# Optimization experiments

Measured on AMD Instinct MI355X. Metric: run time of the kernel, lower is better.

Reference implementation:

```python
import jax, jax.numpy as jnp
import numpy as np

# Sizes
N, E = 100000, 3200000
F_NODE, F_EDGE, LD, HID, L = 4, 4, 6, 16, 8
ALPHA = 1.0
EPS = 1e-6


def setup_inputs() -> dict:
    key = jax.random.key(0)
    ks = jax.random.split(key, 8)
    x = jax.random.normal(ks[0], (N, F_NODE), jnp.float32)
    fixed_mask = jax.random.uniform(ks[1], (N,)) < 0.1
    x = x.at[:, -1].set(jnp.where(fixed_mask, jnp.abs(x[:, -1]) + 1.0, 0.0))
    # positive edge attributes (pipe resistance etc.)
    edge_attr = jax.random.uniform(ks[2], (E, F_EDGE), jnp.float32) * 0.9 + 0.1
    edge_index = jax.random.randint(ks[3], (2, E), 0, N, dtype=jnp.int64)
    d_in = 2 * LD + 2 * F_NODE + F_EDGE  # 24: [x_src, x_dst, attr_src, attr_dst, edge_attr]
    s = 0.1
    W1 = jax.random.normal(ks[4], (L, d_in, HID), jnp.float32) * s
    b1 = jnp.zeros((L, HID), jnp.float32)
    W2 = jax.random.normal(ks[5], (L, HID, LD), jnp.float32) * s
    b2 = jnp.zeros((L, LD), jnp.float32)
    Wf = jax.random.normal(ks[6], (LD, 1), jnp.float32) * s
    bf = jnp.zeros((1,), jnp.float32)
    return {"x": x, "edge_attr": edge_attr, "edge_index": edge_index,
            "W1": W1, "b1": b1, "W2": W2, "b2": b2, "Wf": Wf, "bf": bf}


def reference(x, edge_attr, edge_index, W1, b1, W2, b2, Wf, bf):
    src, dst = edge_index[0], edge_index[1]
    # in-degree for mean aggregation
    deg = jax.ops.segment_sum(jnp.ones((E,), jnp.float32), dst, num_segments=N)
    deg = jnp.maximum(deg, 1.0)
    X = jnp.zeros((N, LD), jnp.float32)
    na_src, na_dst = x[src], x[dst]  # static node-attr gathers reused each layer
    for l in range(L):  # num_convs GNNSConv layers
        m_in = jnp.concatenate([X[src], X[dst], na_src, na_dst, edge_attr], axis=-1)  # [E,24]
        h = jax.nn.relu(m_in @ W1[l] + b1[l])         # per-edge MLP hidden [E,16]
        m = h @ W2[l] + b2[l]                          # per-edge message [E,6]
        agg = jax.ops.segment_sum(m, dst, num_segments=N) / deg[:, None]  # mean aggr
        X = (1.0 - ALPHA) * X + ALPHA * agg            # latent update (alpha_update_x)
        X = jax.nn.relu(X)
    P = jax.nn.relu(X @ Wf + bf)                       # [N,1]
    fixed = x[:, -1]
    P_ = jnp.where(fixed != 0, fixed, P.reshape(-1))   # keep known pressures
    # BalanceConv: gas-network flow from squared-pressure drop, k = edge resistance
    dp2 = P_[src] ** 2 - P_[dst] ** 2
    k = edge_attr[:, 0]
    flows = jnp.sign(dp2) * jnp.sqrt(jnp.abs(dp2) / k + EPS)  # [E]
    inj = x[:, 0]  # nodal injection/demand
    balance = (jax.ops.segment_sum(flows, dst, num_segments=N)
               - jax.ops.segment_sum(flows, src, num_segments=N) + inj)
    imbalance = jnp.sqrt(jnp.sum(balance ** 2))
    return P, flows, jnp.stack([imbalance])
```

## Files before the change

### kernel.cpp

```cpp
#include <hip/hip_runtime.h>
#include <math.h>

#define N_NODES 100000
#define N_EDGES 3200000
#define F_NODE 4
#define F_EDGE 4
#define LD 6
#define HID 16
#define NLAYER 8
#define EPSF 1e-6f

#define NPB 64
#define NBK 1563
#define NBIN 196
#define G1 2000
#define CH (N_EDGES / G1)
#define TILE 2048

__device__ __forceinline__ unsigned f2bf(float a, float b) {
    unsigned ua = __float_as_uint(a);
    ua = (ua + 0x7fffu + ((ua >> 16) & 1u)) >> 16;
    unsigned ub = __float_as_uint(b);
    ub = (ub + 0x7fffu + ((ub >> 16) & 1u)) & 0xffff0000u;
    return ua | ub;
}
__device__ __forceinline__ float bflo(unsigned u) { return __uint_as_float(u << 16); }
__device__ __forceinline__ float bfhi(unsigned u) { return __uint_as_float(u & 0xffff0000u); }

__global__ __launch_bounds__(256) void hist_kernel(const int* __restrict__ ei,
                                                   int* __restrict__ ghd,
                                                   int* __restrict__ ghs) {
    __shared__ int hd[NBIN];
    __shared__ int hs[NBIN];
    int t = threadIdx.x, blk = blockIdx.x;
    for (int i = t; i < NBIN; i += 256) { hd[i] = 0; hs[i] = 0; }
    __syncthreads();
    int beg = blk * CH, end = beg + CH;
    for (int e = beg + t; e < end; e += 256) {
        atomicAdd(&hs[ei[e] >> 9], 1);
        atomicAdd(&hd[ei[N_EDGES + e] >> 9], 1);
    }
    __syncthreads();
    for (int i = t; i < NBIN; i += 256) {
        ghd[(size_t)i * G1 + blk] = hd[i];
        ghs[(size_t)i * G1 + blk] = hs[i];
    }
}

__global__ __launch_bounds__(256) void scanb_kernel(int* __restrict__ ghd, int* __restrict__ ghs,
                                                    int* __restrict__ totd, int* __restrict__ tots) {
    __shared__ int part[256];
    int b = blockIdx.x, t = threadIdx.x;
#pragma unroll
    for (int a = 0; a < 2; a++) {
        int* g = a ? ghs : ghd;
        int vals[8];
        int sum = 0;
#pragma unroll
        for (int k = 0; k < 8; k++) {
            int idx = t * 8 + k;
            vals[k] = (idx < G1) ? g[(size_t)b * G1 + idx] : 0;
            sum += vals[k];
        }
        part[t] = sum;
        __syncthreads();
        for (int off = 1; off < 256; off <<= 1) {
            int v = (t >= off) ? part[t - off] : 0;
            __syncthreads();
            part[t] += v;
            __syncthreads();
        }
        int excl = part[t] - sum;
#pragma unroll
        for (int k = 0; k < 8; k++) {
            int idx = t * 8 + k;
            if (idx < G1) g[(size_t)b * G1 + idx] = excl;
            excl += vals[k];
        }
        if (t == 0) (a ? tots : totd)[b] = part[255];
        __syncthreads();
    }
}

__global__ __launch_bounds__(256) void totscan_kernel(const int* __restrict__ totd,
                                                      const int* __restrict__ tots,
                                                      int* __restrict__ binbased,
                                                      int* __restrict__ binbases) {
    __shared__ int part[256];
    int t = threadIdx.x;
#pragma unroll
    for (int a = 0; a < 2; a++) {
        const int* tot = a ? tots : totd;
        int* base = a ? binbases : binbased;
        int v = (t < NBIN) ? tot[t] : 0;
        part[t] = v;
        __syncthreads();
        for (int off = 1; off < 256; off <<= 1) {
            int u = (t >= off) ? part[t - off] : 0;
            __syncthreads();
            part[t] += u;
            __syncthreads();
        }
        if (t < NBIN) base[t] = part[t] - v;
        if (t == 0) base[NBIN] = N_EDGES;
        __syncthreads();
    }
}

__global__ __launch_bounds__(256) void scatterA_kernel(const int* __restrict__ ei,
                                                       const int* __restrict__ ghd,
                                                       const int* __restrict__ ghs,
                                                       const int* __restrict__ binbased,
                                                       const int* __restrict__ binbases,
                                                       uint2* __restrict__ recA,
                                                       unsigned* __restrict__ sbufA) {
    __shared__ int curd[NBIN];
    __shared__ int curs[NBIN];
    int t = threadIdx.x, blk = blockIdx.x;
    for (int i = t; i < NBIN; i += 256) {
        curd[i] = binbased[i] + ghd[(size_t)i * G1 + blk];
        curs[i] = binbases[i] + ghs[(size_t)i * G1 + blk];
    }
    __syncthreads();
    int beg = blk * CH, end = beg + CH;
    for (int e = beg + t; e < end; e += 256) {
        int s = ei[e], d = ei[N_EDGES + e];
        int p = atomicAdd(&curd[d >> 9], 1);
        recA[p] = make_uint2((unsigned)s | ((unsigned)(d & 511) << 17), (unsigned)e);
        int q = atomicAdd(&curs[s >> 9], 1);
        sbufA[q] = (unsigned)e | ((unsigned)(s & 511) << 22);
    }
}

__global__ __launch_bounds__(256) void sortrec_kernel(const uint2* __restrict__ recA,
                                                      const float* __restrict__ ea,
                                                      const int* __restrict__ binbased,
                                                      uint4* __restrict__ recB,
                                                      float* __restrict__ degInv,
                                                      int* __restrict__ based_bk) {
    __shared__ int hist[512];
    __shared__ int cur[512];
    __shared__ int part[256];
    int b = blockIdx.x, t = threadIdx.x;
    hist[t] = 0;
    hist[t + 256] = 0;
    __syncthreads();
    int beg = binbased[b], end = binbased[b + 1];
    for (int i = beg + t; i < end; i += 256)
        atomicAdd(&hist[(recA[i].x >> 17) & 511u], 1);
    __syncthreads();
    int s0 = hist[2 * t], s1 = hist[2 * t + 1];
    int tsum = s0 + s1;
    part[t] = tsum;
    __syncthreads();
    for (int off = 1; off < 256; off <<= 1) {
        int v = (t >= off) ? part[t - off] : 0;
        __syncthreads();
        part[t] += v;
        __syncthreads();
    }
    int excl = part[t] - tsum;
    cur[2 * t] = beg + excl;
    cur[2 * t + 1] = beg + excl + s0;
    __syncthreads();
    int node0 = b << 9;
    for (int j = t; j < 512; j += 256) {
        int node = node0 + j;
        if (node < N_NODES) degInv[node] = 1.0f / fmaxf((float)hist[j], 1.0f);
    }
    if (t < 8) {
        int node = node0 + t * 64;
        if (node < N_NODES) based_bk[(b << 3) + t] = cur[t * 64];
    }
    if (b == NBIN - 1 && t == 0) based_bk[NBK] = N_EDGES;
    __syncthreads();
    for (int i = beg + t; i < end; i += 256) {
        uint2 r = recA[i];
        int nib = (int)((r.x >> 17) & 511u);
        unsigned s = r.x & 0x1FFFFu;
        unsigned e = r.y;
        int p = atomicAdd(&cur[nib], 1);
        float4 ev = reinterpret_cast<const float4*>(ea)[e];
        recB[p] = make_uint4(s | ((unsigned)(nib & 63) << 17),
                             f2bf(ev.x, ev.y), f2bf(ev.z, ev.w), e);
    }
}

__global__ __launch_bounds__(256) void sortsrc_kernel(const unsigned* __restrict__ sbufA,
                                                      const int* __restrict__ binbases,
                                                      unsigned* __restrict__ sbufB,
                                                      int* __restrict__ bases_bk) {
    __shared__ int hist[512];
    __shared__ int cur[512];
    __shared__ int part[256];
    int b = blockIdx.x, t = threadIdx.x;
    hist[t] = 0;
    hist[t + 256] = 0;
    __syncthreads();
    int beg = binbases[b], end = binbases[b + 1];
    for (int i = beg + t; i < end; i += 256)
        atomicAdd(&hist[(sbufA[i] >> 22) & 511u], 1);
    __syncthreads();
    int s0 = hist[2 * t], s1 = hist[2 * t + 1];
    int tsum = s0 + s1;
    part[t] = tsum;
    __syncthreads();
    for (int off = 1; off < 256; off <<= 1) {
        int v = (t >= off) ? part[t - off] : 0;
        __syncthreads();
        part[t] += v;
        __syncthreads();
    }
    int excl = part[t] - tsum;
    cur[2 * t] = beg + excl;
    cur[2 * t + 1] = beg + excl + s0;
    __syncthreads();
    if (t < 8) {
        int node = (b << 9) + t * 64;
        if (node < N_NODES) bases_bk[(b << 3) + t] = cur[t * 64];
    }
    if (b == NBIN - 1 && t == 0) bases_bk[NBK] = N_EDGES;
    __syncthreads();
    for (int i = beg + t; i < end; i += 256) {
        unsigned w = sbufA[i];
        int nib = (int)((w >> 22) & 511u);
        int p = atomicAdd(&cur[nib], 1);
        sbufB[p] = (w & 0x3FFFFFu) | ((unsigned)(nib & 63) << 22);
    }
}

__global__ __launch_bounds__(256) void ab_init(const float* __restrict__ x,
                                               const float* __restrict__ W1,
                                               const float* __restrict__ b1,
                                               unsigned* __restrict__ A,
                                               unsigned* __restrict__ B) {
    __shared__ float sW[8 * HID];
    __shared__ float sb[HID];
    int t = threadIdx.x;
    for (int i = t; i < 8 * HID; i += 256) sW[i] = W1[12 * HID + i];
    if (t < HID) sb[t] = b1[t];
    __syncthreads();
    int i = blockIdx.x * 256 + t;
    if (i >= N_NODES) return;
    float4 xv = reinterpret_cast<const float4*>(x)[i];
    float xf[4] = {xv.x, xv.y, xv.z, xv.w};
    float a[HID], bb[HID];
#pragma unroll
    for (int j = 0; j < HID; j++) { a[j] = sb[j]; bb[j] = 0.0f; }
#pragma unroll
    for (int r = 0; r < 4; r++) {
        float v = xf[r];
#pragma unroll
        for (int j = 0; j < HID; j++) {
            a[j]  = fmaf(v, sW[r * HID + j], a[j]);
            bb[j] = fmaf(v, sW[(4 + r) * HID + j], bb[j]);
        }
    }
    uint4* Ao = reinterpret_cast<uint4*>(A + (size_t)i * 8);
    Ao[0] = make_uint4(f2bf(a[0], a[1]), f2bf(a[2], a[3]), f2bf(a[4], a[5]), f2bf(a[6], a[7]));
    Ao[1] = make_uint4(f2bf(a[8], a[9]), f2bf(a[10], a[11]), f2bf(a[12], a[13]), f2bf(a[14], a[15]));
    uint4* Bo = reinterpret_cast<uint4*>(B + (size_t)i * 8);
    Bo[0] = make_uint4(f2bf(bb[0], bb[1]), f2bf(bb[2], bb[3]), f2bf(bb[4], bb[5]), f2bf(bb[6], bb[7]));
    Bo[1] = make_uint4(f2bf(bb[8], bb[9]), f2bf(bb[10], bb[11]), f2bf(bb[12], bb[13]), f2bf(bb[14], bb[15]));
}

template <int LAST>
__global__ __launch_bounds__(256) void edge_layer(const uint4* __restrict__ recB,
                                                  const unsigned* __restrict__ Ain,
                                                  const unsigned* __restrict__ Bin,
                                                  const float* __restrict__ x,
                                                  const float* __restrict__ degInv,
                                                  const float* __restrict__ W1l,
                                                  const float* __restrict__ W2l,
                                                  const float* __restrict__ b2l,
                                                  const float* __restrict__ W1n,
                                                  const float* __restrict__ b1n,
                                                  const float* __restrict__ Wf,
                                                  const float* __restrict__ bfp,
                                                  const int* __restrict__ based_bk,
                                                  unsigned* __restrict__ Aout,
                                                  unsigned* __restrict__ Bout,
                                                  float* __restrict__ Pout,
                                                  float* __restrict__ Pbuf) {
    __shared__ float sWea[4 * HID];
    __shared__ float sW2[HID * LD];
    __shared__ float sb2[LD];
    __shared__ float sW1n[20 * HID];
    __shared__ float sb1n[HID];
    __shared__ float sWf[LD];
    __shared__ float sbf;
    __shared__ float accf[LD * NPB];
    __shared__ unsigned sB[NPB * 8];
    __shared__ uint4 tile[TILE];
    int t = threadIdx.x;
    int b = blockIdx.x;
    for (int i = t; i < 4 * HID; i += 256) sWea[i] = W1l[20 * HID + i];
    for (int i = t; i < HID * LD; i += 256) sW2[i] = W2l[i];
    if (t < LD) sb2[t] = b2l[t];
    if (!LAST) {
        for (int i = t; i < 20 * HID; i += 256) sW1n[i] = W1n[i];
        if (t < HID) sb1n[t] = b1n[t];
    } else {
        if (t < LD) sWf[t] = Wf[t];
        if (t == 0) sbf = bfp[0];
    }
    for (int i = t; i < LD * NPB; i += 256) accf[i] = 0.0f;
    {
        size_t base8 = (size_t)(b << 6) * 8;
        for (int i = t; i < NPB * 8; i += 256) {
            size_t gi = base8 + i;
            sB[i] = (gi < (size_t)N_NODES * 8) ? Bin[gi] : 0u;
        }
    }
    __syncthreads();

    int beg = based_bk[b], end = based_bk[b + 1];

    for (int base = beg; base < end; base += TILE) {
        int m = end - base;
        if (m > TILE) m = TILE;
        for (int i = t; i < m; i += 256) tile[i] = recB[base + i];
        __syncthreads();
        int K2 = (m + 255) >> 8;
        int q0 = t * K2;
        int q1 = q0 + K2;
        if (q1 > m) q1 = m;
        float acc[LD];
        int cur = -1;
        uint4 bx, by;
#pragma unroll
        for (int o = 0; o < LD; o++) acc[o] = 0.0f;
#pragma unroll 2
        for (int q = q0; q < q1; ++q) {
            uint4 r = tile[q];
            int dl = (int)((r.x >> 17) & 63u);
            if (dl != cur) {
                if (cur >= 0) {
#pragma unroll
                    for (int o = 0; o < LD; o++) atomicAdd(&accf[o * NPB + cur], acc[o]);
                }
                cur = dl;
#pragma unroll
                for (int o = 0; o < LD; o++) acc[o] = 0.0f;
                const uint4* Bp = reinterpret_cast<const uint4*>(sB) + dl * 2;
                bx = Bp[0];
                by = Bp[1];
            }
            int s = (int)(r.x & 0x1FFFFu);
            const uint4* Ap = reinterpret_cast<const uint4*>(Ain + (size_t)s * 8);
            uint4 ax = Ap[0], ay = Ap[1];
            float h[HID];
            h[0]  = bflo(ax.x) + bflo(bx.x);  h[1]  = bfhi(ax.x) + bfhi(bx.x);
            h[2]  = bflo(ax.y) + bflo(bx.y);  h[3]  = bfhi(ax.y) + bfhi(bx.y);
            h[4]  = bflo(ax.z) + bflo(bx.z);  h[5]  = bfhi(ax.z) + bfhi(bx.z);
            h[6]  = bflo(ax.w) + bflo(bx.w);  h[7]  = bfhi(ax.w) + bfhi(bx.w);
            h[8]  = bflo(ay.x) + bflo(by.x);  h[9]  = bfhi(ay.x) + bfhi(by.x);
            h[10] = bflo(ay.y) + bflo(by.y);  h[11] = bfhi(ay.y) + bfhi(by.y);
            h[12] = bflo(ay.z) + bflo(by.z);  h[13] = bfhi(ay.z) + bfhi(by.z);
            h[14] = bflo(ay.w) + bflo(by.w);  h[15] = bfhi(ay.w) + bfhi(by.w);
            float ef[4] = {bflo(r.y), bfhi(r.y), bflo(r.z), bfhi(r.z)};
#pragma unroll
            for (int rr = 0; rr < 4; rr++) {
                float v = ef[rr];
#pragma unroll
                for (int j = 0; j < HID; j++) h[j] = fmaf(v, sWea[rr * HID + j], h[j]);
            }
#pragma unroll
            for (int j = 0; j < HID; j++) h[j] = fmaxf(h[j], 0.0f);
            float mo[LD];
#pragma unroll
            for (int o = 0; o < LD; o++) mo[o] = sb2[o];
#pragma unroll
            for (int j = 0; j < HID; j++) {
                float hj = h[j];
#pragma unroll
                for (int o = 0; o < LD; o++) mo[o] = fmaf(hj, sW2[j * LD + o], mo[o]);
            }
#pragma unroll
            for (int o = 0; o < LD; o++) acc[o] += mo[o];
        }
        if (cur >= 0) {
#pragma unroll
            for (int o = 0; o < LD; o++) atomicAdd(&accf[o * NPB + cur], acc[o]);
        }
        __syncthreads();
    }

    if (t < NPB) {
        int gid = (b << 6) + t;
        if (gid < N_NODES) {
            float inv = degInv[gid];
            float Xv[LD];
#pragma unroll
            for (int o = 0; o < LD; o++) Xv[o] = fmaxf(accf[o * NPB + t] * inv, 0.0f);
            if (LAST) {
                float a2 = sbf;
#pragma unroll
                for (int o = 0; o < LD; o++) a2 = fmaf(Xv[o], sWf[o], a2);
                float P = fmaxf(a2, 0.0f);
                Pout[gid] = P;
                float fx = x[gid * F_NODE + 3];
                Pbuf[gid] = (fx != 0.0f) ? fx : P;
            } else {
                float4 xv = reinterpret_cast<const float4*>(x)[gid];
                float xf[4] = {xv.x, xv.y, xv.z, xv.w};
                float a[HID], bb[HID];
#pragma unroll
                for (int j = 0; j < HID; j++) { a[j] = sb1n[j]; bb[j] = 0.0f; }
#pragma unroll
                for (int rr = 0; rr < LD; rr++) {
                    float v = Xv[rr];
#pragma unroll
                    for (int j = 0; j < HID; j++) {
                        a[j]  = fmaf(v, sW1n[rr * HID + j], a[j]);
                        bb[j] = fmaf(v, sW1n[(LD + rr) * HID + j], bb[j]);
                    }
                }
#pragma unroll
                for (int rr = 0; rr < 4; rr++) {
                    float v = xf[rr];
#pragma unroll
                    for (int j = 0; j < HID; j++) {
                        a[j]  = fmaf(v, sW1n[(12 + rr) * HID + j], a[j]);
                        bb[j] = fmaf(v, sW1n[(16 + rr) * HID + j], bb[j]);
                    }
                }
                uint4* Ao = reinterpret_cast<uint4*>(Aout + (size_t)gid * 8);
                Ao[0] = make_uint4(f2bf(a[0], a[1]), f2bf(a[2], a[3]), f2bf(a[4], a[5]), f2bf(a[6], a[7]));
                Ao[1] = make_uint4(f2bf(a[8], a[9]), f2bf(a[10], a[11]), f2bf(a[12], a[13]), f2bf(a[14], a[15]));
                uint4* Bo = reinterpret_cast<uint4*>(Bout + (size_t)gid * 8);
                Bo[0] = make_uint4(f2bf(bb[0], bb[1]), f2bf(bb[2], bb[3]), f2bf(bb[4], bb[5]), f2bf(bb[6], bb[7]));
                Bo[1] = make_uint4(f2bf(bb[8], bb[9]), f2bf(bb[10], bb[11]), f2bf(bb[12], bb[13]), f2bf(bb[14], bb[15]));
            }
        }
    }
}

__global__ __launch_bounds__(256) void flows_noatomic(const int* __restrict__ ei,
                                                      const float* __restrict__ ea,
                                                      const float* __restrict__ Pbuf,
                                                      float* __restrict__ flows_out) {
    int e = blockIdx.x * 256 + threadIdx.x;
    if (e >= N_EDGES) return;
    int s = ei[e];
    int d = ei[N_EDGES + e];
    float ps = Pbuf[s], pd = Pbuf[d];
    float dp2 = ps * ps - pd * pd;
    float k = ea[(size_t)e * F_EDGE];
    float sg = (dp2 > 0.0f) ? 1.0f : ((dp2 < 0.0f) ? -1.0f : 0.0f);
    flows_out[e] = sg * sqrtf(fabsf(dp2) / k + EPSF);
}

__global__ __launch_bounds__(256) void balance_in(const uint4* __restrict__ recB,
                                                  const float* __restrict__ flows,
                                                  const float* __restrict__ x,
                                                  const int* __restrict__ based_bk,
                                                  float* __restrict__ bal) {
    __shared__ float acc[NPB];
    int t = threadIdx.x;
    if (t < NPB) acc[t] = 0.0f;
    __syncthreads();
    int b = blockIdx.x;
    int beg = based_bk[b], end = based_bk[b + 1];
    int lane = t & 63;
    for (int base = beg; base < end; base += 256) {
        int p = base + t;
        bool valid = p < end;
        int key = -1;
        float f = 0.0f;
        if (valid) {
            uint4 r = recB[p];
            key = (int)((r.x >> 17) & 63u);
            f = flows[r.w];
        }
#pragma unroll
        for (int st = 1; st < 64; st <<= 1) {
            int kup = __shfl_up(key, st, 64);
            float v = __shfl_up(f, st, 64);
            if ((lane >= st) && (kup == key)) f += v;
        }
        int knx = __shfl_down(key, 1, 64);
        bool tail = (lane == 63) || (knx != key);
        if (valid && tail) atomicAdd(&acc[key], f);
    }
    __syncthreads();
    if (t < NPB) {
        int gid = (b << 6) + t;
        if (gid < N_NODES) bal[gid] = acc[t] + x[gid * F_NODE + 0];
    }
}

__global__ __launch_bounds__(256) void balance_out(const unsigned* __restrict__ sbufB,
                                                   const float* __restrict__ flows,
                                                   const int* __restrict__ bases_bk,
                                                   const float* __restrict__ bal,
                                                   float* __restrict__ imb2) {
    __shared__ float acc[NPB];
    int t = threadIdx.x;
    if (t < NPB) acc[t] = 0.0f;
    __syncthreads();
    int b = blockIdx.x;
    int beg = bases_bk[b], end = bases_bk[b + 1];
    int lane = t & 63;
    for (int base = beg; base < end; base += 256) {
        int q = base + t;
        bool valid = q < end;
        int key = -1;
        float f = 0.0f;
        if (valid) {
            unsigned u = sbufB[q];
            key = (int)((u >> 22) & 63u);
            f = flows[u & 0x3FFFFFu];
        }
#pragma unroll
        for (int st = 1; st < 64; st <<= 1) {
            int kup = __shfl_up(key, st, 64);
            float v = __shfl_up(f, st, 64);
            if ((lane >= st) && (kup == key)) f += v;
        }
        int knx = __shfl_down(key, 1, 64);
        bool tail = (lane == 63) || (knx != key);
        if (valid && tail) atomicAdd(&acc[key], f);
    }
    __syncthreads();
    if (t < NPB) {
        float v = 0.0f;
        int gid = (b << 6) + t;
        if (gid < N_NODES) {
            float bv = bal[gid] - acc[t];
            v = bv * bv;
        }
#pragma unroll
        for (int off = 32; off > 0; off >>= 1) v += __shfl_down(v, off, 64);
        if (t == 0) atomicAdd(imb2, v);
    }
}

__global__ void fin_kernel(const float* __restrict__ imb2, float* __restrict__ out) {
    out[0] = sqrtf(imb2[0]);
}

extern "C" void kernel_launch(void* const* d_in, const int* in_sizes, int n_in,
                              void* d_out, int out_size, void* d_ws, size_t ws_size,
                              hipStream_t stream) {
    const float* x   = (const float*)d_in[0];
    const float* ea  = (const float*)d_in[1];
    const int*   ei  = (const int*)d_in[2];
    const float* W1  = (const float*)d_in[3];
    const float* b1  = (const float*)d_in[4];
    const float* W2  = (const float*)d_in[5];
    const float* b2  = (const float*)d_in[6];
    const float* Wf  = (const float*)d_in[7];
    const float* bf_ = (const float*)d_in[8];
    float* out = (float*)d_out;

    const size_t N = N_NODES, E = N_EDGES;

    size_t o = 0;
    auto alloc = [&](size_t n) { size_t r = o; o += (n + 3) & ~(size_t)3; return r; };
    size_t o_recB     = alloc(4 * E);
    size_t o_recA     = alloc(2 * E);
    size_t o_sbufA    = alloc(E);
    size_t o_ghd      = alloc((size_t)NBIN * G1);
    size_t o_ghs      = alloc((size_t)NBIN * G1);
    size_t o_totd     = alloc(NBIN);
    size_t o_tots     = alloc(NBIN);
    size_t o_binbased = alloc(NBIN + 1);
    size_t o_binbases = alloc(NBIN + 1);
    size_t o_basedbk  = alloc(NBK + 1);
    size_t o_basesbk  = alloc(NBK + 1);
    size_t o_degInv   = alloc(N);
    size_t o_A0       = alloc(8 * N);
    size_t o_B0       = alloc(8 * N);
    size_t o_A1       = alloc(8 * N);
    size_t o_B1       = alloc(8 * N);
    size_t o_Pbuf     = alloc(N);
    size_t o_bal      = alloc(N);
    size_t o_imb2     = alloc(16);
    (void)o;

    int* wsi = (int*)d_ws;
    uint4*    recB     = (uint4*)(wsi + o_recB);
    uint2*    recA     = (uint2*)(wsi + o_recA);
    unsigned* sbufA    = (unsigned*)(wsi + o_sbufA);
    unsigned* sbufB    = (unsigned*)(wsi + o_recA);
    int*      ghd      = wsi + o_ghd;
    int*      ghs      = wsi + o_ghs;
    int*      totd     = wsi + o_totd;
    int*      tots     = wsi + o_tots;
    int*      binbased = wsi + o_binbased;
    int*      binbases = wsi + o_binbases;
    int*      based_bk = wsi + o_basedbk;
    int*      bases_bk = wsi + o_basesbk;
    float*    degInv   = (float*)(wsi + o_degInv);
    unsigned* A0       = (unsigned*)(wsi + o_A0);
    unsigned* B0       = (unsigned*)(wsi + o_B0);
    unsigned* A1       = (unsigned*)(wsi + o_A1);
    unsigned* B1       = (unsigned*)(wsi + o_B1);
    float*    Pbuf     = (float*)(wsi + o_Pbuf);
    float*    bal      = (float*)(wsi + o_bal);
    float*    imb2     = (float*)(wsi + o_imb2);

    const int NB = (N_NODES + 255) / 256;
    const int EB = (N_EDGES + 255) / 256;

    hipMemsetAsync(imb2, 0, sizeof(float), stream);

    hist_kernel<<<G1, 256, 0, stream>>>(ei, ghd, ghs);
    scanb_kernel<<<NBIN, 256, 0, stream>>>(ghd, ghs, totd, tots);
    totscan_kernel<<<1, 256, 0, stream>>>(totd, tots, binbased, binbases);
    scatterA_kernel<<<G1, 256, 0, stream>>>(ei, ghd, ghs, binbased, binbases, recA, sbufA);
    sortrec_kernel<<<NBIN, 256, 0, stream>>>(recA, ea, binbased, recB, degInv, based_bk);
    sortsrc_kernel<<<NBIN, 256, 0, stream>>>(sbufA, binbases, sbufB, bases_bk);

    ab_init<<<NB, 256, 0, stream>>>(x, W1, b1, A0, B0);

    for (int l = 0; l < NLAYER; l++) {
        const unsigned* Ain = (l & 1) ? A1 : A0;
        const unsigned* Bin = (l & 1) ? B1 : B0;
        unsigned* Aout = (l & 1) ? A0 : A1;
        unsigned* Bout = (l & 1) ? B0 : B1;
        const float* W1l = W1 + (size_t)l * 24 * HID;
        const float* W2l = W2 + (size_t)l * HID * LD;
        const float* b2l = b2 + (size_t)l * LD;
        if (l < NLAYER - 1) {
            edge_layer<0><<<NBK, 256, 0, stream>>>(recB, Ain, Bin, x, degInv, W1l, W2l, b2l,
                                                   W1 + (size_t)(l + 1) * 24 * HID,
                                                   b1 + (size_t)(l + 1) * HID,
                                                   Wf, bf_, based_bk,
                                                   Aout, Bout, out, Pbuf);
        } else {
            edge_layer<1><<<NBK, 256, 0, stream>>>(recB, Ain, Bin, x, degInv, W1l, W2l, b2l,
                                                   W1, b1, Wf, bf_, based_bk,
                                                   Aout, Bout, out, Pbuf);
        }
    }

    flows_noatomic<<<EB, 256, 0, stream>>>(ei, ea, Pbuf, out + N);
    balance_in<<<NBK, 256, 0, stream>>>(recB, out + N, x, based_bk, bal);
    balance_out<<<NBK, 256, 0, stream>>>(sbufB, out + N, bases_bk, bal, imb2);
    fin_kernel<<<1, 1, 0, stream>>>(imb2, out + (size_t)N + E);
}
```

Measured before the change: 944.2 us.

## Split edge records into SoA arrays, parallelize sort passes, use wave segmented reduction

Edge records become three separate 32-bit arrays (source/dst-local key plus two bf16-packed attribute words), and the edge index field is dropped. Edge attributes are packed during the first scatter, so the second sort pass no longer gathers them. Both sort passes are split into separate histogram and scatter kernels with four blocks per bin for more parallelism, and G1 is halved. The edge layer drops its shared-memory tile and per-thread run accumulation in favour of a direct coalesced load plus a wave-level segmented shuffle reduction. balance_in now recomputes flows from Pbuf instead of gathering the stored flows by edge id. These changes add kernel launches and extra shuffle work per edge.

```diff
diff --git a/kernel.cpp b/kernel.cpp
--- a/kernel.cpp
+++ b/kernel.cpp
@@ -13,9 +13,10 @@
 #define NPB 64
 #define NBK 1563
 #define NBIN 196
-#define G1 2000
+#define G1 1000
 #define CH (N_EDGES / G1)
-#define TILE 2048
+#define SPLIT 4
+#define NSB (NBIN * SPLIT)
 
 __device__ __forceinline__ unsigned f2bf(float a, float b) {
     unsigned ua = __float_as_uint(a);
@@ -54,11 +55,11 @@
 #pragma unroll
     for (int a = 0; a < 2; a++) {
         int* g = a ? ghs : ghd;
-        int vals[8];
+        int vals[4];
         int sum = 0;
 #pragma unroll
-        for (int k = 0; k < 8; k++) {
-            int idx = t * 8 + k;
+        for (int k = 0; k < 4; k++) {
+            int idx = t * 4 + k;
             vals[k] = (idx < G1) ? g[(size_t)b * G1 + idx] : 0;
             sum += vals[k];
         }
@@ -72,8 +73,8 @@
         }
         int excl = part[t] - sum;
 #pragma unroll
-        for (int k = 0; k < 8; k++) {
-            int idx = t * 8 + k;
+        for (int k = 0; k < 4; k++) {
+            int idx = t * 4 + k;
             if (idx < G1) g[(size_t)b * G1 + idx] = excl;
             excl += vals[k];
         }
@@ -108,11 +109,14 @@
 }
 
 __global__ __launch_bounds__(256) void scatterA_kernel(const int* __restrict__ ei,
+                                                       const float* __restrict__ ea,
                                                        const int* __restrict__ ghd,
                                                        const int* __restrict__ ghs,
                                                        const int* __restrict__ binbased,
                                                        const int* __restrict__ binbases,
-                                                       uint2* __restrict__ recA,
+                                                       unsigned* __restrict__ aw0,
+                                                       unsigned* __restrict__ aw1,
+                                                       unsigned* __restrict__ aw2,
                                                        unsigned* __restrict__ sbufA) {
     __shared__ int curd[NBIN];
     __shared__ int curs[NBIN];
@@ -125,32 +129,62 @@
     int beg = blk * CH, end = beg + CH;
     for (int e = beg + t; e < end; e += 256) {
         int s = ei[e], d = ei[N_EDGES + e];
+        float4 ev = reinterpret_cast<const float4*>(ea)[e];
         int p = atomicAdd(&curd[d >> 9], 1);
-        recA[p] = make_uint2((unsigned)s | ((unsigned)(d & 511) << 17), (unsigned)e);
+        aw0[p] = (unsigned)s | ((unsigned)(d & 511) << 17);
+        aw1[p] = f2bf(ev.x, ev.y);
+        aw2[p] = f2bf(ev.z, ev.w);
         int q = atomicAdd(&curs[s >> 9], 1);
         sbufA[q] = (unsigned)e | ((unsigned)(s & 511) << 22);
     }
 }
 
-__global__ __launch_bounds__(256) void sortrec_kernel(const uint2* __restrict__ recA,
-                                                      const float* __restrict__ ea,
-                                                      const int* __restrict__ binbased,
-                                                      uint4* __restrict__ recB,
-                                                      float* __restrict__ degInv,
-                                                      int* __restrict__ based_bk) {
+__global__ __launch_bounds__(256) void sr_hist(const unsigned* __restrict__ aw0,
+                                               const int* __restrict__ binbased,
+                                               int* __restrict__ srh) {
     __shared__ int hist[512];
+    int bs = blockIdx.x, t = threadIdx.x;
+    int b = bs >> 2, h = bs & 3;
+    hist[t] = 0; hist[t + 256] = 0;
+    __syncthreads();
+    int beg = binbased[b], end = binbased[b + 1];
+    int len = end - beg;
+    int p0 = beg + (int)((long long)len * h / SPLIT);
+    int p1 = beg + (int)((long long)len * (h + 1) / SPLIT);
+    for (int i = p0 + t; i < p1; i += 256)
+        atomicAdd(&hist[(aw0[i] >> 17) & 511u], 1);
+    __syncthreads();
+    int* g = srh + (size_t)bs * 512;
+    g[t] = hist[t];
+    g[t + 256] = hist[t + 256];
+}
+
+__global__ __launch_bounds__(256) void sr_scat(const unsigned* __restrict__ aw0,
+                                               const unsigned* __restrict__ aw1,
+                                               const unsigned* __restrict__ aw2,
+                                               const int* __restrict__ binbased,
+                                               const int* __restrict__ srh,
+                                               unsigned* __restrict__ bw0,
+                                               unsigned* __restrict__ bw1,
+                                               unsigned* __restrict__ bw2,
+                                               float* __restrict__ degInv,
+                                               int* __restrict__ based_bk) {
     __shared__ int cur[512];
     __shared__ int part[256];
-    int b = blockIdx.x, t = threadIdx.x;
-    hist[t] = 0;
-    hist[t + 256] = 0;
-    __syncthreads();
+    int bs = blockIdx.x, t = threadIdx.x;
+    int b = bs >> 2, h = bs & 3;
     int beg = binbased[b], end = binbased[b + 1];
-    for (int i = beg + t; i < end; i += 256)
-        atomicAdd(&hist[(recA[i].x >> 17) & 511u], 1);
-    __syncthreads();
-    int s0 = hist[2 * t], s1 = hist[2 * t + 1];
-    int tsum = s0 + s1;
+    int j0 = 2 * t, j1 = 2 * t + 1;
+    int tot0 = 0, tot1 = 0, own0 = 0, own1 = 0;
+    const int* gb = srh + (size_t)(b << 2) * 512;
+#pragma unroll
+    for (int hh = 0; hh < SPLIT; hh++) {
+        int v0 = gb[hh * 512 + j0];
+        int v1 = gb[hh * 512 + j1];
+        if (hh < h) { own0 += v0; own1 += v1; }
+        tot0 += v0; tot1 += v1;
+    }
+    int tsum = tot0 + tot1;
     part[t] = tsum;
     __syncthreads();
     for (int off = 1; off < 256; off <<= 1) {
@@ -160,49 +194,74 @@
         __syncthreads();
     }
     int excl = part[t] - tsum;
-    cur[2 * t] = beg + excl;
-    cur[2 * t + 1] = beg + excl + s0;
-    __syncthreads();
-    int node0 = b << 9;
-    for (int j = t; j < 512; j += 256) {
-        int node = node0 + j;
-        if (node < N_NODES) degInv[node] = 1.0f / fmaxf((float)hist[j], 1.0f);
-    }
-    if (t < 8) {
-        int node = node0 + t * 64;
-        if (node < N_NODES) based_bk[(b << 3) + t] = cur[t * 64];
-    }
-    if (b == NBIN - 1 && t == 0) based_bk[NBK] = N_EDGES;
-    __syncthreads();
-    for (int i = beg + t; i < end; i += 256) {
-        uint2 r = recA[i];
-        int nib = (int)((r.x >> 17) & 511u);
-        unsigned s = r.x & 0x1FFFFu;
-        unsigned e = r.y;
+    cur[j0] = beg + excl + own0;
+    cur[j1] = beg + excl + tot0 + own1;
+    if (h == 0) {
+        int node0 = b << 9;
+        if (node0 + j0 < N_NODES) degInv[node0 + j0] = 1.0f / fmaxf((float)tot0, 1.0f);
+        if (node0 + j1 < N_NODES) degInv[node0 + j1] = 1.0f / fmaxf((float)tot1, 1.0f);
+        if ((t & 31) == 0) {
+            int k = t >> 5;
+            int node = node0 + (k << 6);
+            if (node < N_NODES) based_bk[(b << 3) + k] = beg + excl;
+        }
+        if (b == NBIN - 1 && t == 0) based_bk[NBK] = N_EDGES;
+    }
+    __syncthreads();
+    int len = end - beg;
+    int p0 = beg + (int)((long long)len * h / SPLIT);
+    int p1 = beg + (int)((long long)len * (h + 1) / SPLIT);
+    for (int i = p0 + t; i < p1; i += 256) {
+        unsigned r0 = aw0[i];
+        int nib = (int)((r0 >> 17) & 511u);
         int p = atomicAdd(&cur[nib], 1);
-        float4 ev = reinterpret_cast<const float4*>(ea)[e];
-        recB[p] = make_uint4(s | ((unsigned)(nib & 63) << 17),
-                             f2bf(ev.x, ev.y), f2bf(ev.z, ev.w), e);
-    }
-}
-
-__global__ __launch_bounds__(256) void sortsrc_kernel(const unsigned* __restrict__ sbufA,
-                                                      const int* __restrict__ binbases,
-                                                      unsigned* __restrict__ sbufB,
-                                                      int* __restrict__ bases_bk) {
+        bw0[p] = (r0 & 0x1FFFFu) | ((unsigned)(nib & 63) << 17);
+        bw1[p] = aw1[i];
+        bw2[p] = aw2[i];
+    }
+}
+
+__global__ __launch_bounds__(256) void ss_hist(const unsigned* __restrict__ sbufA,
+                                               const int* __restrict__ binbases,
+                                               int* __restrict__ ssh) {
     __shared__ int hist[512];
+    int bs = blockIdx.x, t = threadIdx.x;
+    int b = bs >> 2, h = bs & 3;
+    hist[t] = 0; hist[t + 256] = 0;
+    __syncthreads();
+    int beg = binbases[b], end = binbases[b + 1];
+    int len = end - beg;
+    int p0 = beg + (int)((long long)len * h / SPLIT);
+    int p1 = beg + (int)((long long)len * (h + 1) / SPLIT);
+    for (int i = p0 + t; i < p1; i += 256)
+        atomicAdd(&hist[(sbufA[i] >> 22) & 511u], 1);
+    __syncthreads();
+    int* g = ssh + (size_t)bs * 512;
+    g[t] = hist[t];
+    g[t + 256] = hist[t + 256];
+}
+
+__global__ __launch_bounds__(256) void ss_scat(const unsigned* __restrict__ sbufA,
+                                               const int* __restrict__ binbases,
+                                               const int* __restrict__ ssh,
+                                               unsigned* __restrict__ sbufB,
+                                               int* __restrict__ bases_bk) {
     __shared__ int cur[512];
     __shared__ int part[256];
-    int b = blockIdx.x, t = threadIdx.x;
-    hist[t] = 0;
-    hist[t + 256] = 0;
-    __syncthreads();
+    int bs = blockIdx.x, t = threadIdx.x;
+    int b = bs >> 2, h = bs & 3;
     int beg = binbases[b], end = binbases[b + 1];
-    for (int i = beg + t; i < end; i += 256)
-        atomicAdd(&hist[(sbufA[i] >> 22) & 511u], 1);
-    __syncthreads();
-    int s0 = hist[2 * t], s1 = hist[2 * t + 1];
-    int tsum = s0 + s1;
+    int j0 = 2 * t, j1 = 2 * t + 1;
+    int tot0 = 0, tot1 = 0, own0 = 0, own1 = 0;
+    const int* gb = ssh + (size_t)(b << 2) * 512;
+#pragma unroll
+    for (int hh = 0; hh < SPLIT; hh++) {
+        int v0 = gb[hh * 512 + j0];
+        int v1 = gb[hh * 512 + j1];
+        if (hh < h) { own0 += v0; own1 += v1; }
+        tot0 += v0; tot1 += v1;
+    }
+    int tsum = tot0 + tot1;
     part[t] = tsum;
     __syncthreads();
     for (int off = 1; off < 256; off <<= 1) {
@@ -212,16 +271,21 @@
         __syncthreads();
     }
     int excl = part[t] - tsum;
-    cur[2 * t] = beg + excl;
-    cur[2 * t + 1] = beg + excl + s0;
-    __syncthreads();
-    if (t < 8) {
-        int node = (b << 9) + t * 64;
-        if (node < N_NODES) bases_bk[(b << 3) + t] = cur[t * 64];
-    }
-    if (b == NBIN - 1 && t == 0) bases_bk[NBK] = N_EDGES;
-    __syncthreads();
-    for (int i = beg + t; i < end; i += 256) {
+    cur[j0] = beg + excl + own0;
+    cur[j1] = beg + excl + tot0 + own1;
+    if (h == 0) {
+        if ((t & 31) == 0) {
+            int k = t >> 5;
+            int node = (b << 9) + (k << 6);
+            if (node < N_NODES) bases_bk[(b << 3) + k] = beg + excl;
+        }
+        if (b == NBIN - 1 && t == 0) bases_bk[NBK] = N_EDGES;
+    }
+    __syncthreads();
+    int len = end - beg;
+    int p0 = beg + (int)((long long)len * h / SPLIT);
+    int p1 = beg + (int)((long long)len * (h + 1) / SPLIT);
+    for (int i = p0 + t; i < p1; i += 256) {
         unsigned w = sbufA[i];
         int nib = (int)((w >> 22) & 511u);
         int p = atomicAdd(&cur[nib], 1);
@@ -265,7 +329,9 @@
 }
 
 template <int LAST>
-__global__ __launch_bounds__(256) void edge_layer(const uint4* __restrict__ recB,
+__global__ __launch_bounds__(256) void edge_layer(const unsigned* __restrict__ bw0,
+                                                  const unsigned* __restrict__ bw1,
+                                                  const unsigned* __restrict__ bw2,
                                                   const unsigned* __restrict__ Ain,
                                                   const unsigned* __restrict__ Bin,
                                                   const float* __restrict__ x,
@@ -291,7 +357,6 @@
     __shared__ float sbf;
     __shared__ float accf[LD * NPB];
     __shared__ unsigned sB[NPB * 8];
-    __shared__ uint4 tile[TILE];
     int t = threadIdx.x;
     int b = blockIdx.x;
     for (int i = t; i < 4 * HID; i += 256) sWea[i] = W1l[20 * HID + i];
@@ -315,40 +380,26 @@
     __syncthreads();
 
     int beg = based_bk[b], end = based_bk[b + 1];
-
-    for (int base = beg; base < end; base += TILE) {
-        int m = end - base;
-        if (m > TILE) m = TILE;
-        for (int i = t; i < m; i += 256) tile[i] = recB[base + i];
-        __syncthreads();
-        int K2 = (m + 255) >> 8;
-        int q0 = t * K2;
-        int q1 = q0 + K2;
-        if (q1 > m) q1 = m;
-        float acc[LD];
-        int cur = -1;
-        uint4 bx, by;
-#pragma unroll
-        for (int o = 0; o < LD; o++) acc[o] = 0.0f;
-#pragma unroll 2
-        for (int q = q0; q < q1; ++q) {
-            uint4 r = tile[q];
-            int dl = (int)((r.x >> 17) & 63u);
-            if (dl != cur) {
-                if (cur >= 0) {
-#pragma unroll
-                    for (int o = 0; o < LD; o++) atomicAdd(&accf[o * NPB + cur], acc[o]);
-                }
-                cur = dl;
-#pragma unroll
-                for (int o = 0; o < LD; o++) acc[o] = 0.0f;
-                const uint4* Bp = reinterpret_cast<const uint4*>(sB) + dl * 2;
-                bx = Bp[0];
-                by = Bp[1];
-            }
-            int s = (int)(r.x & 0x1FFFFu);
+    int lane = t & 63;
+
+    for (int base = beg; base < end; base += 256) {
+        int p = base + t;
+        bool valid = p < end;
+        int key = -1;
+        float out[LD];
+#pragma unroll
+        for (int o = 0; o < LD; o++) out[o] = 0.0f;
+
+        if (valid) {
+            unsigned r0 = bw0[p];
+            unsigned w1 = bw1[p];
+            unsigned w2 = bw2[p];
+            int s = (int)(r0 & 0x1FFFFu);
+            key = (int)((r0 >> 17) & 63u);
             const uint4* Ap = reinterpret_cast<const uint4*>(Ain + (size_t)s * 8);
             uint4 ax = Ap[0], ay = Ap[1];
+            const uint4* Bp = reinterpret_cast<const uint4*>(sB) + key * 2;
+            uint4 bx = Bp[0], by = Bp[1];
             float h[HID];
             h[0]  = bflo(ax.x) + bflo(bx.x);  h[1]  = bfhi(ax.x) + bfhi(bx.x);
             h[2]  = bflo(ax.y) + bflo(bx.y);  h[3]  = bfhi(ax.y) + bfhi(bx.y);
@@ -358,7 +409,7 @@
             h[10] = bflo(ay.y) + bflo(by.y);  h[11] = bfhi(ay.y) + bfhi(by.y);
             h[12] = bflo(ay.z) + bflo(by.z);  h[13] = bfhi(ay.z) + bfhi(by.z);
             h[14] = bflo(ay.w) + bflo(by.w);  h[15] = bfhi(ay.w) + bfhi(by.w);
-            float ef[4] = {bflo(r.y), bfhi(r.y), bflo(r.z), bfhi(r.z)};
+            float ef[4] = {bflo(w1), bfhi(w1), bflo(w2), bfhi(w2)};
 #pragma unroll
             for (int rr = 0; rr < 4; rr++) {
                 float v = ef[rr];
@@ -367,24 +418,34 @@
             }
 #pragma unroll
             for (int j = 0; j < HID; j++) h[j] = fmaxf(h[j], 0.0f);
-            float mo[LD];
-#pragma unroll
-            for (int o = 0; o < LD; o++) mo[o] = sb2[o];
+#pragma unroll
+            for (int o = 0; o < LD; o++) out[o] = sb2[o];
 #pragma unroll
             for (int j = 0; j < HID; j++) {
                 float hj = h[j];
 #pragma unroll
-                for (int o = 0; o < LD; o++) mo[o] = fmaf(hj, sW2[j * LD + o], mo[o]);
+                for (int o = 0; o < LD; o++) out[o] = fmaf(hj, sW2[j * LD + o], out[o]);
             }
-#pragma unroll
-            for (int o = 0; o < LD; o++) acc[o] += mo[o];
-        }
-        if (cur >= 0) {
-#pragma unroll
-            for (int o = 0; o < LD; o++) atomicAdd(&accf[o * NPB + cur], acc[o]);
-        }
-        __syncthreads();
-    }
+        }
+
+#pragma unroll
+        for (int st = 1; st < 64; st <<= 1) {
+            int kup = __shfl_up(key, st, 64);
+            bool same = (lane >= st) && (kup == key);
+#pragma unroll
+            for (int o = 0; o < LD; o++) {
+                float v = __shfl_up(out[o], st, 64);
+                if (same) out[o] += v;
+            }
+        }
+        int knx = __shfl_down(key, 1, 64);
+        bool tail = (lane == 63) || (knx != key);
+        if (valid && tail) {
+#pragma unroll
+            for (int o = 0; o < LD; o++) atomicAdd(&accf[o * NPB + key], out[o]);
+        }
+    }
+    __syncthreads();
 
     if (t < NPB) {
         int gid = (b << 6) + t;
@@ -451,16 +512,22 @@
     flows_out[e] = sg * sqrtf(fabsf(dp2) / k + EPSF);
 }
 
-__global__ __launch_bounds__(256) void balance_in(const uint4* __restrict__ recB,
-                                                  const float* __restrict__ flows,
+__global__ __launch_bounds__(256) void balance_in(const unsigned* __restrict__ bw0,
+                                                  const unsigned* __restrict__ bw1,
+                                                  const float* __restrict__ Pbuf,
                                                   const float* __restrict__ x,
                                                   const int* __restrict__ based_bk,
                                                   float* __restrict__ bal) {
     __shared__ float acc[NPB];
+    __shared__ float pdl[NPB];
     int t = threadIdx.x;
-    if (t < NPB) acc[t] = 0.0f;
-    __syncthreads();
     int b = blockIdx.x;
+    if (t < NPB) {
+        acc[t] = 0.0f;
+        int gid = (b << 6) + t;
+        pdl[t] = (gid < N_NODES) ? Pbuf[gid] : 0.0f;
+    }
+    __syncthreads();
     int beg = based_bk[b], end = based_bk[b + 1];
     int lane = t & 63;
     for (int base = beg; base < end; base += 256) {
@@ -469,9 +536,15 @@
         int key = -1;
         float f = 0.0f;
         if (valid) {
-            uint4 r = recB[p];
-            key = (int)((r.x >> 17) & 63u);
-            f = flows[r.w];
+            unsigned r0 = bw0[p];
+            int s = (int)(r0 & 0x1FFFFu);
+            key = (int)((r0 >> 17) & 63u);
+            float ps = Pbuf[s];
+            float pd = pdl[key];
+            float k = bflo(bw1[p]);
+            float dp2 = ps * ps - pd * pd;
+            float sg = (dp2 > 0.0f) ? 1.0f : ((dp2 < 0.0f) ? -1.0f : 0.0f);
+            f = sg * sqrtf(fabsf(dp2) / k + EPSF);
         }
 #pragma unroll
         for (int st = 1; st < 64; st <<= 1) {
@@ -558,11 +631,17 @@
 
     size_t o = 0;
     auto alloc = [&](size_t n) { size_t r = o; o += (n + 3) & ~(size_t)3; return r; };
-    size_t o_recB     = alloc(4 * E);
-    size_t o_recA     = alloc(2 * E);
+    size_t o_bw0      = alloc(E);
+    size_t o_bw1      = alloc(E);
+    size_t o_bw2      = alloc(E);
+    size_t o_aw0      = alloc(E);
+    size_t o_aw1      = alloc(E);
+    size_t o_aw2      = alloc(E);
     size_t o_sbufA    = alloc(E);
     size_t o_ghd      = alloc((size_t)NBIN * G1);
     size_t o_ghs      = alloc((size_t)NBIN * G1);
+    size_t o_srh      = alloc((size_t)NSB * 512);
+    size_t o_ssh      = alloc((size_t)NSB * 512);
     size_t o_totd     = alloc(NBIN);
     size_t o_tots     = alloc(NBIN);
     size_t o_binbased = alloc(NBIN + 1);
@@ -580,12 +659,18 @@
     (void)o;
 
     int* wsi = (int*)d_ws;
-    uint4*    recB     = (uint4*)(wsi + o_recB);
-    uint2*    recA     = (uint2*)(wsi + o_recA);
+    unsigned* bw0      = (unsigned*)(wsi + o_bw0);
+    unsigned* bw1      = (unsigned*)(wsi + o_bw1);
+    unsigned* bw2      = (unsigned*)(wsi + o_bw2);
+    unsigned* aw0      = (unsigned*)(wsi + o_aw0);
+    unsigned* aw1      = (unsigned*)(wsi + o_aw1);
+    unsigned* aw2      = (unsigned*)(wsi + o_aw2);
     unsigned* sbufA    = (unsigned*)(wsi + o_sbufA);
-    unsigned* sbufB    = (unsigned*)(wsi + o_recA);
+    unsigned* sbufB    = (unsigned*)(wsi + o_aw0);
     int*      ghd      = wsi + o_ghd;
     int*      ghs      = wsi + o_ghs;
+    int*      srh      = wsi + o_srh;
+    int*      ssh      = wsi + o_ssh;
     int*      totd     = wsi + o_totd;
     int*      tots     = wsi + o_tots;
     int*      binbased = wsi + o_binbased;
@@ -609,9 +694,13 @@
     hist_kernel<<<G1, 256, 0, stream>>>(ei, ghd, ghs);
     scanb_kernel<<<NBIN, 256, 0, stream>>>(ghd, ghs, totd, tots);
     totscan_kernel<<<1, 256, 0, stream>>>(totd, tots, binbased, binbases);
-    scatterA_kernel<<<G1, 256, 0, stream>>>(ei, ghd, ghs, binbased, binbases, recA, sbufA);
-    sortrec_kernel<<<NBIN, 256, 0, stream>>>(recA, ea, binbased, recB, degInv, based_bk);
-    sortsrc_kernel<<<NBIN, 256, 0, stream>>>(sbufA, binbases, sbufB, bases_bk);
+    scatterA_kernel<<<G1, 256, 0, stream>>>(ei, ea, ghd, ghs, binbased, binbases,
+                                            aw0, aw1, aw2, sbufA);
+    sr_hist<<<NSB, 256, 0, stream>>>(aw0, binbased, srh);
+    sr_scat<<<NSB, 256, 0, stream>>>(aw0, aw1, aw2, binbased, srh,
+                                     bw0, bw1, bw2, degInv, based_bk);
+    ss_hist<<<NSB, 256, 0, stream>>>(sbufA, binbases, ssh);
+    ss_scat<<<NSB, 256, 0, stream>>>(sbufA, binbases, ssh, sbufB, bases_bk);
 
     ab_init<<<NB, 256, 0, stream>>>(x, W1, b1, A0, B0);
 
@@ -624,20 +713,22 @@
         const float* W2l = W2 + (size_t)l * HID * LD;
         const float* b2l = b2 + (size_t)l * LD;
         if (l < NLAYER - 1) {
-            edge_layer<0><<<NBK, 256, 0, stream>>>(recB, Ain, Bin, x, degInv, W1l, W2l, b2l,
+            edge_layer<0><<<NBK, 256, 0, stream>>>(bw0, bw1, bw2, Ain, Bin, x, degInv,
+                                                   W1l, W2l, b2l,
                                                    W1 + (size_t)(l + 1) * 24 * HID,
                                                    b1 + (size_t)(l + 1) * HID,
                                                    Wf, bf_, based_bk,
                                                    Aout, Bout, out, Pbuf);
         } else {
-            edge_layer<1><<<NBK, 256, 0, stream>>>(recB, Ain, Bin, x, degInv, W1l, W2l, b2l,
+            edge_layer<1><<<NBK, 256, 0, stream>>>(bw0, bw1, bw2, Ain, Bin, x, degInv,
+                                                   W1l, W2l, b2l,
                                                    W1, b1, Wf, bf_, based_bk,
                                                    Aout, Bout, out, Pbuf);
         }
     }
 
     flows_noatomic<<<EB, 256, 0, stream>>>(ei, ea, Pbuf, out + N);
-    balance_in<<<NBK, 256, 0, stream>>>(recB, out + N, x, based_bk, bal);
+    balance_in<<<NBK, 256, 0, stream>>>(bw0, bw1, Pbuf, x, based_bk, bal);
     balance_out<<<NBK, 256, 0, stream>>>(sbufB, out + N, bases_bk, bal, imb2);
     fin_kernel<<<1, 1, 0, stream>>>(imb2, out + (size_t)N + E);
 }
```

Result: no change. 961.6 us (+1.8%).
